# Kernel tuning notes

Hardware: AMD Instinct MI355X
Metric: run time of the kernel (lower is better)

Reference implementation:

```python
import jax, jax.numpy as jnp
import numpy as np

EMB = 1024
HEADS = 16
DH = EMB // HEADS
EPS = 1e-5


def _layernorm(x, w, b):
    mean = jnp.mean(x, axis=-1, keepdims=True)
    var = jnp.mean((x - mean) ** 2, axis=-1, keepdims=True)  # unbiased=False
    return w * (x - mean) / jnp.sqrt(var + EPS) + b


def _gelu_tanh(x):
    c = jnp.sqrt(jnp.asarray(2.0 / jnp.pi, x.dtype))
    return 0.5 * x * (1.0 + jnp.tanh(c * (x + 0.044715 * x ** 3)))


def setup_inputs() -> dict:
    key = jax.random.key(0)
    ks = jax.random.split(key, 8)
    B, N = 2, 2048
    s = lambda fan_in: 1.0 / np.sqrt(fan_in)
    # weights stored as [in, out] (torch Linear applied as x @ W.T == x @ W_here)
    return {
        "x": jax.random.normal(ks[0], (B, N, EMB), jnp.float32),
        "ln1_w": jnp.ones((EMB,), jnp.float32),
        "ln1_b": jnp.zeros((EMB,), jnp.float32),
        "w_qkv": jax.random.normal(ks[1], (EMB, 3 * EMB), jnp.float32) * s(EMB),  # qkv_bias=False
        "w_attn_proj": jax.random.normal(ks[2], (EMB, EMB), jnp.float32) * s(EMB),
        "b_attn_proj": jnp.zeros((EMB,), jnp.float32),
        "ln2_w": jnp.ones((EMB,), jnp.float32),
        "ln2_b": jnp.zeros((EMB,), jnp.float32),
        "w_fc": jax.random.normal(ks[3], (EMB, 4 * EMB), jnp.float32) * s(EMB),
        "b_fc": jnp.zeros((4 * EMB,), jnp.float32),
        "w_proj": jax.random.normal(ks[4], (4 * EMB, EMB), jnp.float32) * s(4 * EMB),
        "b_proj": jnp.zeros((EMB,), jnp.float32),
    }


def reference(x, ln1_w, ln1_b, w_qkv, w_attn_proj, b_attn_proj,
              ln2_w, ln2_b, w_fc, b_fc, w_proj, b_proj):
    B, N, _ = x.shape
    # --- attention sublayer (pre-LN) ---
    h = _layernorm(x, ln1_w, ln1_b)
    qkv = h @ w_qkv  # [B,N,3E]
    q, k, v = jnp.split(qkv, 3, axis=-1)
    # [B,H,N,Dh]
    q = q.reshape(B, N, HEADS, DH).transpose(0, 2, 1, 3)
    k = k.reshape(B, N, HEADS, DH).transpose(0, 2, 1, 3)
    v = v.reshape(B, N, HEADS, DH).transpose(0, 2, 1, 3)
    scores = jnp.einsum("bhqd,bhkd->bhqk", q, k) * (DH ** -0.5)
    causal = jnp.tril(jnp.ones((N, N), bool))
    scores = jnp.where(causal, scores, -jnp.inf)
    attn = jax.nn.softmax(scores, axis=-1)  # attn_pdrop=0 (eval)
    ctx = jnp.einsum("bhqk,bhkd->bhqd", attn, v)
    ctx = ctx.transpose(0, 2, 1, 3).reshape(B, N, EMB)
    x = x + (ctx @ w_attn_proj + b_attn_proj)  # resid_pdrop=0
    # --- MLP sublayer (pre-LN) ---
    h = _layernorm(x, ln2_w, ln2_b)
    h = _gelu_tanh(h @ w_fc + b_fc)
    x = x + (h @ w_proj + b_proj)
    return x
```

## Files before the change

### kernel.cpp

```cpp
#include <hip/hip_runtime.h>
#include <stdint.h>

#define EMB 1024
#define NHEAD 16
#define DH 64
#define SEQ 2048
#define NTOK 4096

typedef __attribute__((ext_vector_type(8))) short s16x8;
typedef __attribute__((ext_vector_type(4))) short s16x4;
typedef __attribute__((ext_vector_type(4))) float f32x4;
typedef __attribute__((ext_vector_type(4))) unsigned short u16x4;

__device__ __forceinline__ unsigned short f2bf(float f){
    union { float f; unsigned int u; } v; v.f = f;
    unsigned int r = v.u + 0x7fffu + ((v.u >> 16) & 1u);
    return (unsigned short)(r >> 16);
}

__device__ __forceinline__ f32x4 mfma16(s16x8 a, s16x8 b, f32x4 c){
    return __builtin_amdgcn_mfma_f32_16x16x32_bf16(a, b, c, 0, 0, 0);
}

__device__ __forceinline__ void gload16(const void* g, void* l){
    __builtin_amdgcn_global_load_lds((const __attribute__((address_space(1))) void*)g,
                                     (__attribute__((address_space(3))) void*)l, 16, 0, 0);
}

__device__ __forceinline__ s16x8 cat8(s16x4 a, s16x4 b){
    s16x8 r;
    r[0]=a[0]; r[1]=a[1]; r[2]=a[2]; r[3]=a[3];
    r[4]=b[0]; r[5]=b[1]; r[6]=b[2]; r[7]=b[3];
    return r;
}

__device__ __forceinline__ unsigned cvtpk(float lo, float hi){
    unsigned r;
    asm("v_cvt_pk_bf16_f32 %0, %1, %2" : "=v"(r) : "v"(lo), "v"(hi));
    return r;
}

__device__ __forceinline__ s16x8 qscale(s16x8 q){
    s16x8 r;
    #pragma unroll
    for (int e = 0; e < 8; ++e){
        union { float f; unsigned u; } v;
        v.u = ((unsigned)(unsigned short)q[e]) << 16;
        v.f *= 0.125f;
        r[e] = (short)f2bf(v.f);
    }
    return r;
}

__global__ __launch_bounds__(256) void convT_kernel(const float* __restrict__ in,
                                                    unsigned short* __restrict__ out,
                                                    int R, int C){
    __shared__ float tile[32][33];
    const int c0 = blockIdx.x * 32, r0 = blockIdx.y * 32;
    const int tx = threadIdx.x, ty = threadIdx.y;
    #pragma unroll
    for (int k = 0; k < 4; ++k)
        tile[ty*4+k][tx] = in[(long)(r0 + ty*4 + k) * C + c0 + tx];
    __syncthreads();
    #pragma unroll
    for (int k = 0; k < 4; ++k)
        out[(long)(c0 + ty*4 + k) * R + r0 + tx] = f2bf(tile[tx][ty*4+k]);
}

__global__ __launch_bounds__(256) void vT_kernel(const unsigned short* __restrict__ qkv,
                                                 unsigned short* __restrict__ vtg){
    __shared__ unsigned short tile[64*64];
    const int bh = blockIdx.y, b = bh >> 4, h = bh & 15;
    const int n0 = blockIdx.x * 64;
    const int t = threadIdx.x;
    const int nr = t >> 3, c0 = (t & 7) * 8;
    #pragma unroll
    for (int hh = 0; hh < 2; ++hh){
        const int n = nr + hh*32;
        uint4 vv = *(const uint4*)&qkv[(long)(b*SEQ + n0 + n)*3072 + 2048 + h*64 + c0];
        *(uint4*)((char*)tile + n*128 + ((c0*2) ^ (((n>>3)&7)<<4))) = vv;
    }
    __syncthreads();
    #pragma unroll
    for (int hh = 0; hh < 2; ++hh){
        const int d = nr + hh*32;
        union { unsigned short u[8]; uint4 v; } tmp;
        #pragma unroll
        for (int j = 0; j < 8; ++j){
            const int n = c0 + j;
            tmp.u[j] = *(const unsigned short*)((char*)tile + n*128 + ((d*2) ^ (((n>>3)&7)<<4)));
        }
        *(uint4*)&vtg[((long)bh*64 + d)*2048 + n0 + c0] = tmp.v;
    }
}

__global__ __launch_bounds__(256) void ln_kernel(const float* __restrict__ x,
                                                 const float* __restrict__ w,
                                                 const float* __restrict__ b,
                                                 unsigned short* __restrict__ out){
    const int row = blockIdx.x, tid = threadIdx.x;
    const float4 v = ((const float4*)(x + (long)row * EMB))[tid];
    float s  = v.x + v.y + v.z + v.w;
    float ss = v.x*v.x + v.y*v.y + v.z*v.z + v.w*v.w;
    #pragma unroll
    for (int off = 32; off >= 1; off >>= 1){
        s  += __shfl_xor(s,  off, 64);
        ss += __shfl_xor(ss, off, 64);
    }
    __shared__ float ps[4], pss[4];
    const int wv = tid >> 6;
    if ((tid & 63) == 0){ ps[wv] = s; pss[wv] = ss; }
    __syncthreads();
    s  = ps[0] + ps[1] + ps[2] + ps[3];
    ss = pss[0] + pss[1] + pss[2] + pss[3];
    const float mean = s * (1.0f/EMB);
    const float var  = ss * (1.0f/EMB) - mean*mean;
    const float rstd = rsqrtf(var + 1e-5f);
    const float4 wv4 = ((const float4*)w)[tid];
    const float4 bv4 = ((const float4*)b)[tid];
    u16x4 o;
    o[0] = f2bf((v.x - mean) * rstd * wv4.x + bv4.x);
    o[1] = f2bf((v.y - mean) * rstd * wv4.y + bv4.y);
    o[2] = f2bf((v.z - mean) * rstd * wv4.z + bv4.z);
    o[3] = f2bf((v.w - mean) * rstd * wv4.w + bv4.w);
    *(u16x4*)(out + (long)row * EMB + tid * 4) = o;
}

__global__ __launch_bounds__(256) void red_kernel(const float* __restrict__ p0,
                                                  const float* __restrict__ p1,
                                                  const float* __restrict__ bias,
                                                  const float* __restrict__ resid,
                                                  float* __restrict__ out, int N){
    const long i = ((long)blockIdx.x * 256 + threadIdx.x) * 4;
    const float4 a = *(const float4*)(p0 + i);
    const float4 b = *(const float4*)(p1 + i);
    const float4 r = *(const float4*)(resid + i);
    const float4 bb = *(const float4*)(bias + ((int)i & (N - 1)));
    float4 o;
    o.x = a.x + b.x + r.x + bb.x;
    o.y = a.y + b.y + r.y + bb.y;
    o.z = a.z + b.z + r.z + bb.z;
    o.w = a.w + b.w + r.w + bb.w;
    *(float4*)(out + i) = o;
}

template<int EPI, int BM, int BN, int WR, int WC, int SK>
__global__ __launch_bounds__(WR*WC*64) void gemm_kernel(const unsigned short* __restrict__ A,
                                                        const unsigned short* __restrict__ Bt,
                                                        const float* __restrict__ bias,
                                                        const float* __restrict__ resid,
                                                        void* __restrict__ out0,
                                                        void* __restrict__ out1,
                                                        int M, int N, int K){
    constexpr int NW = WR * WC;
    constexpr int NT = NW * 64;
    constexpr int FI = BM / (WR * 16);
    constexpr int FJ = BN / (WC * 16);
    __shared__ unsigned short As[2][BM * 32];
    __shared__ unsigned short Bs[2][BN * 32];
    const int tid  = threadIdx.x;
    const int lane = tid & 63, w = tid >> 6;
    const int lm = lane & 15, g = lane >> 4;
    const int wr = w / WC, wc = w % WC;

    const int gx = gridDim.x;
    const int nwg = gx * gridDim.y;
    int id = blockIdx.y * gx + blockIdx.x;
    id = (id & 7) * (nwg >> 3) + (id >> 3);
    const int m0 = (id / gx) * BM, n0 = (id % gx) * BN;
    const int kz = (SK > 1) ? blockIdx.z : 0;
    const int kbase = kz * (K / SK);

    f32x4 zero = {0.0f, 0.0f, 0.0f, 0.0f};
    f32x4 acc[FI][FJ];
    #pragma unroll
    for (int i = 0; i < FI; ++i)
        #pragma unroll
        for (int j = 0; j < FJ; ++j) acc[i][j] = zero;

    auto stage = [&](int kt, int bu){
        #pragma unroll
        for (int p = 0; p < BM/(NT/4); ++p)
            gload16(&A[(long)(m0 + p*(NT/4) + (tid>>2)) * K + kt + (tid&3)*8],
                    (char*)&As[bu][0] + p*(NT*16) + tid*16);
        #pragma unroll
        for (int p = 0; p < BN/(NT/4); ++p)
            gload16(&Bt[(long)(n0 + p*(NT/4) + (tid>>2)) * K + kt + (tid&3)*8],
                    (char*)&Bs[bu][0] + p*(NT*16) + tid*16);
    };

    stage(kbase, 0);
    int cur = 0;
    const int nkt = (K / SK) / 32;
    for (int t = 0; t < nkt; ++t){
        __syncthreads();
        if (t + 1 < nkt) stage(kbase + (t+1)*32, cur ^ 1);
        s16x8 af[FI], bf[FJ];
        #pragma unroll
        for (int i = 0; i < FI; ++i)
            af[i] = *(const s16x8*)&As[cur][(wr*(FI*16) + i*16 + lm)*32 + g*8];
        #pragma unroll
        for (int j = 0; j < FJ; ++j)
            bf[j] = *(const s16x8*)&Bs[cur][(wc*(FJ*16) + j*16 + lm)*32 + g*8];
        #pragma unroll
        for (int i = 0; i < FI; ++i)
            #pragma unroll
            for (int j = 0; j < FJ; ++j)
                acc[i][j] = mfma16(af[i], bf[j], acc[i][j]);
        cur ^= 1;
    }

    float* po = (SK > 1 && kz == 1) ? (float*)out1 : (float*)out0;
    #pragma unroll
    for (int i = 0; i < FI; ++i){
        #pragma unroll
        for (int r = 0; r < 4; ++r){
            const int row = m0 + wr*(FI*16) + i*16 + 4*g + r;
            #pragma unroll
            for (int j = 0; j < FJ; ++j){
                const int col = n0 + wc*(FJ*16) + j*16 + lm;
                const float v = acc[i][j][r];
                if (EPI == 0){
                    ((unsigned short*)out0)[(long)row * N + col] = f2bf(v);
                } else if (EPI == 1){
                    ((float*)out0)[(long)row * N + col] =
                        v + bias[col] + resid[(long)row * N + col];
                } else if (EPI == 2){
                    const float xx = v + bias[col];
                    const float z = 0.7978845608f * (xx + 0.044715f * xx * xx * xx);
                    const float gg = xx / (1.0f + __expf(-2.0f * z));
                    ((unsigned short*)out0)[(long)row * N + col] = f2bf(gg);
                } else {
                    po[(long)row * N + col] = v;
                }
            }
        }
    }
}

__global__ __launch_bounds__(256) void attn_kernel(const unsigned short* __restrict__ qkv,
                                                   const unsigned short* __restrict__ vtg,
                                                   unsigned short* __restrict__ ctx){
    __shared__ unsigned short Ks[2][4096];
    __shared__ unsigned short Vs[2][4096];
    const int pair = blockIdx.x, bh = blockIdx.y;
    const int b = bh >> 4, h = bh & 15;
    const int tid = threadIdx.x, lane = tid & 63, w = tid >> 6;
    const int lm = lane & 15, g = lane >> 4;
    const long qkvb = (long)b * SEQ * 3072;
    const unsigned short* kglob = qkv + qkvb + 1024 + h*64;
    const unsigned short* vglob = vtg + (long)bh * 64 * 2048;

    const int srow = tid >> 3;
    const int soff = (tid & 7) * 16;
    f32x4 zero = {0.0f, 0.0f, 0.0f, 0.0f};

    #pragma unroll 1
    for (int grp = 0; grp < 2; ++grp){
        const int qg = (grp == 0) ? pair : (31 - pair);
        const int q0 = qg * 64;
        const int nt = qg + 1;
        const int qrow = q0 + w*16 + lm;

        const unsigned short* qrp = qkv + qkvb + (long)qrow*3072 + h*64;
        const s16x8 qf0 = qscale(*(const s16x8*)(qrp + g*8));
        const s16x8 qf1 = qscale(*(const s16x8*)(qrp + 32 + g*8));

        f32x4 o[4];
        #pragma unroll
        for (int d = 0; d < 4; ++d) o[d] = zero;
        float mrun = -3e38f, lrun = 0.0f;

        auto stage = [&](int t, int bu){
            const int kv0 = t * 64;
            #pragma unroll
            for (int hh = 0; hh < 2; ++hh){
                const int row = srow + hh*32;
                const int sw  = soff ^ ((row & 7) << 4);
                gload16(kglob + (long)(kv0 + row)*3072 + (sw >> 1),
                        (char*)&Ks[bu][0] + hh*4096 + w*1024);
                gload16(vglob + (long)row*2048 + kv0 + (sw >> 1),
                        (char*)&Vs[bu][0] + hh*4096 + w*1024);
            }
        };

        __syncthreads();
        stage(0, 0);
        int cur = 0;
        #pragma unroll 1
        for (int t = 0; t < nt; ++t){
            __syncthreads();
            if (t + 1 < nt) stage(t + 1, cur ^ 1);

            const char* Kb = (const char*)&Ks[cur][0];
            const int sw = (lm & 7) << 4;
            f32x4 sc[4];
            #pragma unroll
            for (int s = 0; s < 4; ++s){
                const char* rp = Kb + (s*16 + lm)*128;
                s16x8 kf0 = *(const s16x8*)(rp + ((g*16) ^ sw));
                s16x8 kf1 = *(const s16x8*)(rp + ((64 + g*16) ^ sw));
                f32x4 a = mfma16(kf0, qf0, zero);
                sc[s] = mfma16(kf1, qf1, a);
            }

            const bool diag = (t == nt - 1);
            float p[4][4];
            float mx = -3e38f;
            #pragma unroll
            for (int s = 0; s < 4; ++s)
                #pragma unroll
                for (int r = 0; r < 4; ++r){
                    float vv = sc[s][r];
                    if (diag && (s*16 + 4*g + r > w*16 + lm)) vv = -3e38f;
                    p[s][r] = vv;
                    mx = fmaxf(mx, vv);
                }
            mx = fmaxf(mx, __shfl_xor(mx, 16, 64));
            mx = fmaxf(mx, __shfl_xor(mx, 32, 64));
            if (!__all(mx - mrun <= 8.0f)){
                const float mnew = fmaxf(mrun, mx);
                const float corr = __expf(mrun - mnew);
                lrun *= corr;
                #pragma unroll
                for (int d = 0; d < 4; ++d) o[d] *= corr;
                mrun = mnew;
            }
            float rs = 0.0f;
            #pragma unroll
            for (int s = 0; s < 4; ++s)
                #pragma unroll
                for (int r = 0; r < 4; ++r){
                    const float e = __expf(p[s][r] - mrun);
                    p[s][r] = e;
                    rs += e;
                }
            rs += __shfl_xor(rs, 16, 64);
            rs += __shfl_xor(rs, 32, 64);
            lrun += rs;

            union { unsigned u[4]; s16x8 v; } P0, P1;
            P0.u[0] = cvtpk(p[0][0], p[0][1]);
            P0.u[1] = cvtpk(p[0][2], p[0][3]);
            P0.u[2] = cvtpk(p[1][0], p[1][1]);
            P0.u[3] = cvtpk(p[1][2], p[1][3]);
            P1.u[0] = cvtpk(p[2][0], p[2][1]);
            P1.u[1] = cvtpk(p[2][2], p[2][3]);
            P1.u[2] = cvtpk(p[3][0], p[3][1]);
            P1.u[3] = cvtpk(p[3][2], p[3][3]);

            const char* Vb = (const char*)&Vs[cur][0];
            #pragma unroll
            for (int d = 0; d < 4; ++d){
                const char* vrp = Vb + (d*16 + lm)*128;
                s16x4 a0 = *(const s16x4*)(vrp + ((g*8) ^ sw));
                s16x4 a1 = *(const s16x4*)(vrp + ((32 + g*8) ^ sw));
                o[d] = mfma16(cat8(a0, a1), P0.v, o[d]);
                s16x4 b0 = *(const s16x4*)(vrp + ((64 + g*8) ^ sw));
                s16x4 b1 = *(const s16x4*)(vrp + ((96 + g*8) ^ sw));
                o[d] = mfma16(cat8(b0, b1), P1.v, o[d]);
            }
            cur ^= 1;
        }

        const float inv = 1.0f / lrun;
        unsigned short* cw = ctx + (long)(b*SEQ + qrow)*EMB + h*DH + 4*g;
        #pragma unroll
        for (int d = 0; d < 4; ++d){
            u16x4 ov;
            ov[0] = f2bf(o[d][0]*inv); ov[1] = f2bf(o[d][1]*inv);
            ov[2] = f2bf(o[d][2]*inv); ov[3] = f2bf(o[d][3]*inv);
            *(u16x4*)(cw + d*16) = ov;
        }
    }
}

extern "C" void kernel_launch(void* const* d_in, const int* in_sizes, int n_in,
                              void* d_out, int out_size, void* d_ws, size_t ws_size,
                              hipStream_t stream){
    const float* x     = (const float*)d_in[0];
    const float* ln1_w = (const float*)d_in[1];
    const float* ln1_b = (const float*)d_in[2];
    const float* w_qkv = (const float*)d_in[3];
    const float* w_ap  = (const float*)d_in[4];
    const float* b_ap  = (const float*)d_in[5];
    const float* ln2_w = (const float*)d_in[6];
    const float* ln2_b = (const float*)d_in[7];
    const float* w_fc  = (const float*)d_in[8];
    const float* b_fc  = (const float*)d_in[9];
    const float* w_pr  = (const float*)d_in[10];
    const float* b_pr  = (const float*)d_in[11];
    float* out = (float*)d_out;

    char* ws = (char*)d_ws;
    unsigned short* wqkvT = (unsigned short*)(ws + 0);
    unsigned short* wapT  = (unsigned short*)(ws + 6291456);
    unsigned short* wfcT  = (unsigned short*)(ws + 8388608);
    unsigned short* wprT  = (unsigned short*)(ws + 16777216);
    unsigned short* h1    = (unsigned short*)(ws + 25165824);
    unsigned short* vtg   = (unsigned short*)(ws + 25165824);
    unsigned short* qkv   = (unsigned short*)(ws + 33554432);
    unsigned short* ctx   = (unsigned short*)(ws + 58720256);
    float*          x1    = (float*)(ws + 67108864);
    unsigned short* h2    = (unsigned short*)(ws + 83886080);
    unsigned short* afc   = (unsigned short*)(ws + 92274688);
    float* pp0 = (float*)(ws + 0);
    float* pp1 = (float*)(ws + 25165824);

    dim3 b32(32, 8, 1);
    convT_kernel<<<dim3(3072/32, 1024/32), b32, 0, stream>>>(w_qkv, wqkvT, 1024, 3072);
    convT_kernel<<<dim3(1024/32, 1024/32), b32, 0, stream>>>(w_ap,  wapT,  1024, 1024);
    convT_kernel<<<dim3(4096/32, 1024/32), b32, 0, stream>>>(w_fc,  wfcT,  1024, 4096);
    convT_kernel<<<dim3(1024/32, 4096/32), b32, 0, stream>>>(w_pr,  wprT,  4096, 1024);

    ln_kernel<<<NTOK, 256, 0, stream>>>(x, ln1_w, ln1_b, h1);

    gemm_kernel<0,128,128,2,2,1><<<dim3(3072/128, NTOK/128), 256, 0, stream>>>(
        h1, wqkvT, nullptr, nullptr, qkv, nullptr, NTOK, 3072, 1024);

    vT_kernel<<<dim3(SEQ/64, 32), 256, 0, stream>>>(qkv, vtg);

    attn_kernel<<<dim3(16, 32), 256, 0, stream>>>(qkv, vtg, ctx);

    gemm_kernel<1,128,64,2,2,1><<<dim3(1024/64, NTOK/128), 256, 0, stream>>>(
        ctx, wapT, b_ap, x, x1, nullptr, NTOK, 1024, 1024);

    ln_kernel<<<NTOK, 256, 0, stream>>>(x1, ln2_w, ln2_b, h2);

    gemm_kernel<2,128,128,2,2,1><<<dim3(4096/128, NTOK/128), 256, 0, stream>>>(
        h2, wfcT, b_fc, nullptr, afc, nullptr, NTOK, 4096, 1024);

    gemm_kernel<3,128,64,2,1,2><<<dim3(1024/64, NTOK/128, 2), 128, 0, stream>>>(
        afc, wprT, nullptr, nullptr, pp0, pp1, NTOK, 1024, 4096);
    red_kernel<<<NTOK*EMB/1024, 256, 0, stream>>>(pp0, pp1, b_pr, x1, out, EMB);
}
```

Before: 274.3 us.

## Add 256x128 triple-buffered GEMM kernel for QKV, FC and proj layers

Introduces a new GEMM kernel with 256x128 tiles, 8 waves, BK=64, triple-buffered LDS with XOR swizzle, explicit vmcnt waits, s_setprio around MFMA bursts, and a grouped block-id remap for L2 locality. It replaces the 128x128/128x64 GEMMs for the QKV, FC+GELU and split-K projection. The goal is more data reuse per tile and better overlap of global loads with MFMA. In exchange it uses much more LDS (144KB), runs fewer workgroups, and launches a small grid for the projection (8x16x2), which risks lower occupancy and tail effects.

```diff
diff --git a/kernel.cpp b/kernel.cpp
--- a/kernel.cpp
+++ b/kernel.cpp
@@ -142,6 +142,111 @@
     o.z = a.z + b.z + r.z + bb.z;
     o.w = a.w + b.w + r.w + bb.w;
     *(float4*)(out + i) = o;
+}
+
+template<int EPI, int SK>
+__global__ __launch_bounds__(512, 2) void gemm3_kernel(const unsigned short* __restrict__ A,
+                                                       const unsigned short* __restrict__ Bt,
+                                                       const float* __restrict__ bias,
+                                                       void* __restrict__ out0,
+                                                       void* __restrict__ out1,
+                                                       int M, int N, int K){
+    __shared__ unsigned short As[3][256*64];
+    __shared__ unsigned short Bs[3][128*64];
+    const int tid = threadIdx.x, lane = tid & 63, w = tid >> 6;
+    const int lm = lane & 15, g = lane >> 4;
+    const int wr = w >> 1, wc = w & 1;
+
+    const int gx = gridDim.x;
+    const int nwg = gx * gridDim.y;
+    int id = blockIdx.y * gx + blockIdx.x;
+    id = (id & 7) * (nwg >> 3) + (id >> 3);
+    const int m0 = (id / gx) * 256, n0 = (id % gx) * 128;
+    const int kz = (SK > 1) ? blockIdx.z : 0;
+    const int kbase = kz * (K / SK);
+    const int NK = (K / SK) / 64;
+
+    const int r8 = tid >> 3;
+    const int src = (((tid & 7) * 16) ^ ((r8 & 7) << 4)) >> 1;
+    char* AsB = (char*)&As[0][0];
+    char* BsB = (char*)&Bs[0][0];
+
+    auto stage = [&](int bu, int kt){
+        #pragma unroll
+        for (int p = 0; p < 4; ++p)
+            gload16(&A[(long)(m0 + p*64 + r8) * K + kt + src], AsB + bu*32768 + p*8192 + tid*16);
+        #pragma unroll
+        for (int p = 0; p < 2; ++p)
+            gload16(&Bt[(long)(n0 + p*64 + r8) * K + kt + src], BsB + bu*16384 + p*8192 + tid*16);
+    };
+
+    f32x4 zero = {0.0f, 0.0f, 0.0f, 0.0f};
+    f32x4 acc[4][4];
+    #pragma unroll
+    for (int i = 0; i < 4; ++i)
+        #pragma unroll
+        for (int j = 0; j < 4; ++j) acc[i][j] = zero;
+
+    stage(0, kbase);
+    stage(1, kbase + 64);
+    int bk = 0, bs = 2;
+    const int axor = (lm & 7) << 4;
+    for (int k = 0; k < NK; ++k){
+        if (k + 2 < NK) stage(bs, kbase + (k + 2) * 64);
+        if (k + 3 <= NK)      asm volatile("s_waitcnt vmcnt(12)" ::: "memory");
+        else if (k + 2 <= NK) asm volatile("s_waitcnt vmcnt(6)"  ::: "memory");
+        else                  asm volatile("s_waitcnt vmcnt(0)"  ::: "memory");
+        __builtin_amdgcn_s_barrier();
+        asm volatile("" ::: "memory");
+        const char* Ab = AsB + bk*32768;
+        const char* Bb = BsB + bk*16384;
+        #pragma unroll
+        for (int kk = 0; kk < 2; ++kk){
+            s16x8 af[4], bf[4];
+            #pragma unroll
+            for (int i = 0; i < 4; ++i)
+                af[i] = *(const s16x8*)(Ab + (wr*64 + i*16 + lm)*128 + ((kk*64 + g*16) ^ axor));
+            #pragma unroll
+            for (int j = 0; j < 4; ++j)
+                bf[j] = *(const s16x8*)(Bb + (wc*64 + j*16 + lm)*128 + ((kk*64 + g*16) ^ axor));
+            __builtin_amdgcn_s_setprio(1);
+            #pragma unroll
+            for (int i = 0; i < 4; ++i)
+                #pragma unroll
+                for (int j = 0; j < 4; ++j)
+                    acc[i][j] = mfma16(af[i], bf[j], acc[i][j]);
+            __builtin_amdgcn_s_setprio(0);
+        }
+        asm volatile("" ::: "memory");
+        __builtin_amdgcn_s_barrier();
+        asm volatile("" ::: "memory");
+        bk = (bk + 1 == 3) ? 0 : bk + 1;
+        bs = (bs + 1 == 3) ? 0 : bs + 1;
+    }
+
+    float* po = (SK > 1 && kz == 1) ? (float*)out1 : (float*)out0;
+    #pragma unroll
+    for (int i = 0; i < 4; ++i){
+        #pragma unroll
+        for (int r = 0; r < 4; ++r){
+            const int row = m0 + wr*64 + i*16 + 4*g + r;
+            #pragma unroll
+            for (int j = 0; j < 4; ++j){
+                const int col = n0 + wc*64 + j*16 + lm;
+                const float v = acc[i][j][r];
+                if (EPI == 0){
+                    ((unsigned short*)out0)[(long)row * N + col] = f2bf(v);
+                } else if (EPI == 2){
+                    const float xx = v + bias[col];
+                    const float z = 0.7978845608f * (xx + 0.044715f * xx * xx * xx);
+                    const float gg = xx / (1.0f + __expf(-2.0f * z));
+                    ((unsigned short*)out0)[(long)row * N + col] = f2bf(gg);
+                } else {
+                    po[(long)row * N + col] = v;
+                }
+            }
+        }
+    }
 }
 
 template<int EPI, int BM, int BN, int WR, int WC, int SK>
@@ -415,8 +520,8 @@
 
     ln_kernel<<<NTOK, 256, 0, stream>>>(x, ln1_w, ln1_b, h1);
 
-    gemm_kernel<0,128,128,2,2,1><<<dim3(3072/128, NTOK/128), 256, 0, stream>>>(
-        h1, wqkvT, nullptr, nullptr, qkv, nullptr, NTOK, 3072, 1024);
+    gemm3_kernel<0,1><<<dim3(3072/128, NTOK/256), 512, 0, stream>>>(
+        h1, wqkvT, nullptr, qkv, nullptr, NTOK, 3072, 1024);
 
     vT_kernel<<<dim3(SEQ/64, 32), 256, 0, stream>>>(qkv, vtg);
 
@@ -427,10 +532,10 @@
 
     ln_kernel<<<NTOK, 256, 0, stream>>>(x1, ln2_w, ln2_b, h2);
 
-    gemm_kernel<2,128,128,2,2,1><<<dim3(4096/128, NTOK/128), 256, 0, stream>>>(
-        h2, wfcT, b_fc, nullptr, afc, nullptr, NTOK, 4096, 1024);
-
-    gemm_kernel<3,128,64,2,1,2><<<dim3(1024/64, NTOK/128, 2), 128, 0, stream>>>(
-        afc, wprT, nullptr, nullptr, pp0, pp1, NTOK, 1024, 4096);
+    gemm3_kernel<2,1><<<dim3(4096/128, NTOK/256), 512, 0, stream>>>(
+        h2, wfcT, b_fc, afc, nullptr, NTOK, 4096, 1024);
+
+    gemm3_kernel<3,2><<<dim3(1024/128, NTOK/256, 2), 512, 0, stream>>>(
+        afc, wprT, nullptr, pp0, pp1, NTOK, 1024, 4096);
     red_kernel<<<NTOK*EMB/1024, 256, 0, stream>>>(pp0, pp1, b_pr, x1, out, EMB);
 }
```

Measured after the change: 275.5 us. Within noise of the previous version (+0.4%).
